# Performance work log

Hardware: AMD Instinct MI355X
Metric: run time of the kernel (lower is better)

The kernel has to match this reference:

```python
import jax, jax.numpy as jnp
import numpy as np
import math

D_MODEL = 768
N_HEAD = 12
D_FF = 3072
LN_EPS = 1e-5


def gelu_new(x):
    return 0.5 * x * (1.0 + jnp.tanh(jnp.sqrt(2.0 / jnp.pi) * (x + 0.044715 * x ** 3)))


def layer_norm(x, g, b):
    mu = jnp.mean(x, axis=-1, keepdims=True)
    var = jnp.mean(jnp.square(x - mu), axis=-1, keepdims=True)
    return (x - mu) * jax.lax.rsqrt(var + LN_EPS) * g + b


def setup_inputs() -> dict:
    key = jax.random.key(0)
    ks = jax.random.split(key, 8)
    B, S = 4, 2048
    x = jax.random.normal(ks[0], (B, S, D_MODEL), dtype=jnp.float32)
    # causal look-ahead mask: 1 = attend, 0 = masked
    look_ahead_mask = jnp.tril(jnp.ones((S, S), dtype=jnp.float32))[None, None]
    std = 0.02
    Wqkv = jax.random.normal(ks[1], (D_MODEL, 3 * D_MODEL), dtype=jnp.float32) * std
    bqkv = jnp.zeros((3 * D_MODEL,), dtype=jnp.float32)
    Wo = jax.random.normal(ks[2], (D_MODEL, D_MODEL), dtype=jnp.float32) * std
    bo = jnp.zeros((D_MODEL,), dtype=jnp.float32)
    Wfc = jax.random.normal(ks[3], (D_MODEL, D_FF), dtype=jnp.float32) * std
    bfc = jnp.zeros((D_FF,), dtype=jnp.float32)
    Wpr = jax.random.normal(ks[4], (D_FF, D_MODEL), dtype=jnp.float32) * std
    bpr = jnp.zeros((D_MODEL,), dtype=jnp.float32)
    g1 = jnp.ones((D_MODEL,), dtype=jnp.float32)
    b1 = jnp.zeros((D_MODEL,), dtype=jnp.float32)
    g2 = jnp.ones((D_MODEL,), dtype=jnp.float32)
    b2 = jnp.zeros((D_MODEL,), dtype=jnp.float32)
    return dict(x=x, look_ahead_mask=look_ahead_mask, Wqkv=Wqkv, bqkv=bqkv,
                Wo=Wo, bo=bo, Wfc=Wfc, bfc=bfc, Wpr=Wpr, bpr=bpr,
                g1=g1, b1=b1, g2=g2, b2=b2)


def reference(x, look_ahead_mask, Wqkv, bqkv, Wo, bo, Wfc, bfc, Wpr, bpr, g1, b1, g2, b2):
    B, S, D = x.shape
    dk = D // N_HEAD
    # --- attention sublayer (dropout = identity, eval mode) ---
    nx = layer_norm(x, g1, b1)
    qkv = nx @ Wqkv + bqkv                       # [B,S,3D]
    q, k, v = jnp.split(qkv, 3, axis=-1)
    def heads(t):
        return t.reshape(B, S, N_HEAD, dk).transpose(0, 2, 1, 3)  # [B,H,S,dk]
    q, k, v = heads(q), heads(k), heads(v)
    scores = jnp.einsum('bhqd,bhkd->bhqk', q, k) / jnp.sqrt(jnp.float32(dk))
    scores = scores + (1.0 - look_ahead_mask) * -10000.0
    attn_scores = jax.nn.softmax(scores, axis=-1)  # [B,H,S,S]
    out = jnp.einsum('bhqk,bhkd->bhqd', attn_scores, v)
    out = out.transpose(0, 2, 1, 3).reshape(B, S, D)
    a = out @ Wo + bo
    x = x + a
    # --- MLP sublayer ---
    h = layer_norm(x, g2, b2)
    m = gelu_new(h @ Wfc + bfc) @ Wpr + bpr
    x = x + m
    return (x, attn_scores)
```

## Files before the change

### kernel.cpp

```cpp
#include <hip/hip_runtime.h>
#include <stdint.h>

#define D_MODEL 768
#define NHEAD   12
#define DKH     64
#define SEQ     2048
#define BATCH   4
#define DFF     3072
#define NROWS   (BATCH*SEQ)

typedef __bf16 bf16x8 __attribute__((ext_vector_type(8)));
typedef float  f32x4  __attribute__((ext_vector_type(4)));

__device__ __forceinline__ unsigned short f2bf(float f) {
  union { float f; unsigned int u; } v; v.f = f;
  unsigned int r = v.u + 0x7fffu + ((v.u >> 16) & 1u);
  return (unsigned short)(r >> 16);
}

__device__ __forceinline__ void gl_lds16(const void* g, void* l) {
  __builtin_amdgcn_global_load_lds(
      (__attribute__((address_space(1))) void*)(uintptr_t)g,
      (__attribute__((address_space(3))) void*)(uintptr_t)l, 16, 0, 0);
}

__global__ __launch_bounds__(256) void k_wtrans_all(
    const float* __restrict__ Wqkv, const float* __restrict__ Wo,
    const float* __restrict__ Wfc, const float* __restrict__ Wpr,
    unsigned short* __restrict__ WqkvT, unsigned short* __restrict__ WoT,
    unsigned short* __restrict__ WfcT, unsigned short* __restrict__ WprT) {
  int id = blockIdx.x;
  const float* W; unsigned short* Wt; int K, N, tid;
  if (id < 1728)      { W = Wqkv; Wt = WqkvT; K = 768;  N = 2304; tid = id; }
  else if (id < 2304) { W = Wo;   Wt = WoT;   K = 768;  N = 768;  tid = id - 1728; }
  else if (id < 4608) { W = Wfc;  Wt = WfcT;  K = 768;  N = 3072; tid = id - 2304; }
  else                { W = Wpr;  Wt = WprT;  K = 3072; N = 768;  tid = id - 4608; }
  int ntn = N / 32;
  int n0 = (tid % ntn) * 32, k0 = (tid / ntn) * 32;

  __shared__ float tile[32][33];
  int c = threadIdx.x & 31, r = threadIdx.x >> 5;
#pragma unroll
  for (int i = 0; i < 4; ++i)
    tile[r + i * 8][c] = W[(size_t)(k0 + r + i * 8) * N + n0 + c];
  __syncthreads();
#pragma unroll
  for (int i = 0; i < 4; ++i)
    Wt[(size_t)(n0 + r + i * 8) * K + k0 + c] = f2bf(tile[c][r + i * 8]);
}

__global__ __launch_bounds__(256) void k_ln(const float* __restrict__ x,
                                            const float* __restrict__ g,
                                            const float* __restrict__ bb,
                                            unsigned short* __restrict__ y) {
  int row = blockIdx.x, t = threadIdx.x;
  const float* xr = x + (size_t)row * D_MODEL;
  float v0 = xr[t], v1 = xr[t + 256], v2 = xr[t + 512];
  float s = v0 + v1 + v2;
  float s2 = v0 * v0 + v1 * v1 + v2 * v2;
#pragma unroll
  for (int off = 32; off >= 1; off >>= 1) {
    s  += __shfl_xor(s, off, 64);
    s2 += __shfl_xor(s2, off, 64);
  }
  __shared__ float rs_[4], rs2_[4];
  int w = t >> 6;
  if ((t & 63) == 0) { rs_[w] = s; rs2_[w] = s2; }
  __syncthreads();
  s  = rs_[0] + rs_[1] + rs_[2] + rs_[3];
  s2 = rs2_[0] + rs2_[1] + rs2_[2] + rs2_[3];
  float mu  = s * (1.0f / D_MODEL);
  float var = s2 * (1.0f / D_MODEL) - mu * mu;
  float rstd = rsqrtf(var + 1e-5f);
  unsigned short* yr = y + (size_t)row * D_MODEL;
  yr[t]       = f2bf((v0 - mu) * rstd * g[t]       + bb[t]);
  yr[t + 256] = f2bf((v1 - mu) * rstd * g[t + 256] + bb[t + 256]);
  yr[t + 512] = f2bf((v2 - mu) * rstd * g[t + 512] + bb[t + 512]);
}

#define EPI_QKV 0
#define EPI_WO  1
#define EPI_FC  2
#define EPI_PR  3

template <int EPI>
__global__ __launch_bounds__(256) void k_gemm(
    const unsigned short* __restrict__ A,
    const unsigned short* __restrict__ Bt,
    const float* __restrict__ bias,
    const float* __restrict__ res,
    float* __restrict__ outf,
    unsigned short* __restrict__ outb,
    unsigned short* __restrict__ qo,
    unsigned short* __restrict__ ko,
    unsigned short* __restrict__ vto,
    int K, int N) {
  __shared__ __align__(16) unsigned char smem[36864];
  unsigned short* As = (unsigned short*)smem;
  unsigned short* Bs = (unsigned short*)(smem + 16384);
  int t = threadIdx.x;
  int l = t & 63, w = t >> 6;
  int wm = w >> 1, wn = w & 1;
  int m0 = blockIdx.y * 128, n0 = blockIdx.x * 128;
  int lr = l & 15, lg = l >> 4;

  const f32x4 fz = {0.0f, 0.0f, 0.0f, 0.0f};
  f32x4 acc[4][4];
#pragma unroll
  for (int i = 0; i < 4; ++i)
#pragma unroll
    for (int j = 0; j < 4; ++j) acc[i][j] = fz;

  int arow = t >> 3;
  int aslot = t & 7;
  const unsigned short* Ag = A + (size_t)(m0 + arow) * K + aslot * 8;
  const unsigned short* Bg = Bt + (size_t)(n0 + arow) * K + aslot * 8;
  int ntile = K >> 6;

  for (int kt = 0; kt < ntile; ++kt) {
    const unsigned short* Agk = Ag + kt * 64;
    const unsigned short* Bgk = Bg + kt * 64;
#pragma unroll
    for (int i = 0; i < 4; ++i)
      gl_lds16(Agk + (size_t)i * 32 * K, As + (i * 256 + t) * 8);
#pragma unroll
    for (int i = 0; i < 4; ++i)
      gl_lds16(Bgk + (size_t)i * 32 * K, Bs + (i * 256 + t) * 8);
    __syncthreads();
#pragma unroll
    for (int ks = 0; ks < 2; ++ks) {
      bf16x8 af[4], bf_[4];
#pragma unroll
      for (int i = 0; i < 4; ++i)
        af[i] = *(const bf16x8*)(As + (wm * 64 + i * 16 + lr) * 64 + ks * 32 + lg * 8);
#pragma unroll
      for (int i = 0; i < 4; ++i)
        bf_[i] = *(const bf16x8*)(Bs + (wn * 64 + i * 16 + lr) * 64 + ks * 32 + lg * 8);
#pragma unroll
      for (int i = 0; i < 4; ++i)
#pragma unroll
        for (int j = 0; j < 4; ++j)
          acc[i][j] = __builtin_amdgcn_mfma_f32_16x16x32_bf16(af[i], bf_[j], acc[i][j], 0, 0, 0);
    }
    __syncthreads();
  }

  int mb = m0 + wm * 64;
  int nb = n0 + wn * 64;

  if constexpr (EPI == EPI_WO || EPI == EPI_PR) {
#pragma unroll
    for (int i = 0; i < 4; ++i)
#pragma unroll
      for (int r = 0; r < 4; ++r) {
        int m = mb + i * 16 + 4 * lg + r;
#pragma unroll
        for (int j = 0; j < 4; ++j) {
          int n = nb + j * 16 + lr;
          outf[(size_t)m * D_MODEL + n] = acc[i][j][r] + bias[n] + res[(size_t)m * D_MODEL + n];
        }
      }
  } else if constexpr (EPI == EPI_FC) {
#pragma unroll
    for (int i = 0; i < 4; ++i)
#pragma unroll
      for (int r = 0; r < 4; ++r) {
        int m = mb + i * 16 + 4 * lg + r;
#pragma unroll
        for (int j = 0; j < 4; ++j) {
          int n = nb + j * 16 + lr;
          float u = acc[i][j][r] + bias[n];
          float c = 0.7978845608028654f * (u + 0.044715f * u * u * u);
          float a2 = fabsf(c);
          float e = __expf(-2.0f * a2);
          float th = (1.0f - e) / (1.0f + e);
          th = (c < 0.0f) ? -th : th;
          float gl = 0.5f * u * (1.0f + th);
          outb[(size_t)m * DFF + n] = f2bf(gl);
        }
      }
  } else {
    int region = n0 / 768;
    int b = m0 >> 11;
    if (region < 2) {
      unsigned short* dst = (region == 0) ? qo : ko;
#pragma unroll
      for (int i = 0; i < 4; ++i)
#pragma unroll
        for (int r = 0; r < 4; ++r) {
          int m = mb + i * 16 + 4 * lg + r;
          int s = m & (SEQ - 1);
#pragma unroll
          for (int j = 0; j < 4; ++j) {
            int n = nb + j * 16 + lr;
            int nl = n - region * 768;
            int h = nl >> 6, d = nl & 63;
            dst[(((size_t)(b * NHEAD + h) * SEQ + s) << 6) + d] = f2bf(acc[i][j][r] + bias[n]);
          }
        }
    } else {
      int nl = nb - 1536;
      int h = nl >> 6;
      unsigned short* Tw = (unsigned short*)(smem + w * 9216);
#pragma unroll
      for (int j = 0; j < 4; ++j) {
        int dcol = j * 16 + lr;
        int n = nb + j * 16 + lr;
#pragma unroll
        for (int i = 0; i < 4; ++i)
#pragma unroll
          for (int r = 0; r < 4; ++r)
            Tw[dcol * 72 + i * 16 + 4 * lg + r] = f2bf(acc[i][j][r] + bias[n]);
      }
      __syncthreads();
      int srow = l >> 3, sc = (l & 7) * 8;
      int s0 = mb & (SEQ - 1);
#pragma unroll
      for (int i = 0; i < 8; ++i) {
        int d = i * 8 + srow;
        bf16x8 vv = *(const bf16x8*)(Tw + d * 72 + sc);
        *(bf16x8*)(vto + ((size_t)(b * NHEAD + h) * DKH + d) * SEQ + s0 + sc) = vv;
      }
    }
  }
}

template <int WRITEP>
__global__ __launch_bounds__(256) void k_attn(const unsigned short* __restrict__ q,
                                              const unsigned short* __restrict__ kk,
                                              const unsigned short* __restrict__ vt,
                                              float* __restrict__ lsumbuf,
                                              float* __restrict__ attn,
                                              unsigned short* __restrict__ ao) {
  __shared__ __align__(16) unsigned short Ks[64 * 64];
  __shared__ __align__(16) unsigned short Vts[64 * 64];
  __shared__ __align__(16) unsigned short Pw[4][32 * 72];
  int t = threadIdx.x, l = t & 63, w = t >> 6;
  int lr = l & 15, lg = l >> 4;
  int qt = gridDim.x - 1 - blockIdx.x;
  int bh = blockIdx.y;
  int q0 = qt * 128;
  int qrow0 = q0 + w * 32;
  int kmax = 2 * qt + 1;

  bf16x8 aq[2][2];
#pragma unroll
  for (int m = 0; m < 2; ++m) {
    const unsigned short* qbase = q + ((size_t)bh * SEQ + qrow0 + m * 16 + lr) * DKH;
    aq[m][0] = *(const bf16x8*)(qbase + lg * 8);
    aq[m][1] = *(const bf16x8*)(qbase + 32 + lg * 8);
  }

  const f32x4 fz = {0.0f, 0.0f, 0.0f, 0.0f};
  float lsum[2][4] = {{0.f, 0.f, 0.f, 0.f}, {0.f, 0.f, 0.f, 0.f}};

  for (int kt = 0; kt <= kmax; ++kt) {
#pragma unroll
    for (int i = 0; i < 2; ++i) {
      int lin = i * 256 + t;
      gl_lds16(kk + ((size_t)bh * SEQ + kt * 64 + (lin >> 3)) * DKH + (lin & 7) * 8,
               Ks + lin * 8);
    }
    __syncthreads();
#pragma unroll
    for (int m = 0; m < 2; ++m) {
      f32x4 sacc[4];
#pragma unroll
      for (int f = 0; f < 4; ++f) sacc[f] = fz;
#pragma unroll
      for (int f = 0; f < 4; ++f) {
        bf16x8 bk0 = *(const bf16x8*)(Ks + (f * 16 + lr) * 64 + lg * 8);
        sacc[f] = __builtin_amdgcn_mfma_f32_16x16x32_bf16(aq[m][0], bk0, sacc[f], 0, 0, 0);
        bf16x8 bk1 = *(const bf16x8*)(Ks + (f * 16 + lr) * 64 + 32 + lg * 8);
        sacc[f] = __builtin_amdgcn_mfma_f32_16x16x32_bf16(aq[m][1], bk1, sacc[f], 0, 0, 0);
      }
#pragma unroll
      for (int r = 0; r < 4; ++r) {
        int qg = qrow0 + m * 16 + 4 * lg + r;
        float rsum = 0.f;
#pragma unroll
        for (int f = 0; f < 4; ++f) {
          int ksg = kt * 64 + f * 16 + lr;
          float p = (ksg <= qg) ? __expf(sacc[f][r] * 0.125f) : 0.0f;
          rsum += p;
        }
        rsum += __shfl_xor(rsum, 1, 64);
        rsum += __shfl_xor(rsum, 2, 64);
        rsum += __shfl_xor(rsum, 4, 64);
        rsum += __shfl_xor(rsum, 8, 64);
        lsum[m][r] += rsum;
      }
    }
    __syncthreads();
  }
  float invl[2][4];
#pragma unroll
  for (int m = 0; m < 2; ++m)
#pragma unroll
    for (int r = 0; r < 4; ++r) {
      invl[m][r] = 1.0f / lsum[m][r];
      if (WRITEP == 0 && lr == 0)
        lsumbuf[(size_t)bh * SEQ + qrow0 + m * 16 + 4 * lg + r] = lsum[m][r];
    }

  f32x4 oacc[2][4];
#pragma unroll
  for (int m = 0; m < 2; ++m)
#pragma unroll
    for (int f = 0; f < 4; ++f) oacc[m][f] = fz;

  unsigned short* Pme = Pw[w];
  for (int kt = 0; kt <= kmax; ++kt) {
#pragma unroll
    for (int i = 0; i < 2; ++i) {
      int lin = i * 256 + t;
      gl_lds16(kk + ((size_t)bh * SEQ + kt * 64 + (lin >> 3)) * DKH + (lin & 7) * 8,
               Ks + lin * 8);
      gl_lds16(vt + ((size_t)bh * DKH + (lin >> 3)) * SEQ + kt * 64 + (lin & 7) * 8,
               Vts + lin * 8);
    }
    __syncthreads();
#pragma unroll
    for (int m = 0; m < 2; ++m) {
      f32x4 sacc[4];
#pragma unroll
      for (int f = 0; f < 4; ++f) sacc[f] = fz;
#pragma unroll
      for (int f = 0; f < 4; ++f) {
        bf16x8 bk0 = *(const bf16x8*)(Ks + (f * 16 + lr) * 64 + lg * 8);
        sacc[f] = __builtin_amdgcn_mfma_f32_16x16x32_bf16(aq[m][0], bk0, sacc[f], 0, 0, 0);
        bf16x8 bk1 = *(const bf16x8*)(Ks + (f * 16 + lr) * 64 + 32 + lg * 8);
        sacc[f] = __builtin_amdgcn_mfma_f32_16x16x32_bf16(aq[m][1], bk1, sacc[f], 0, 0, 0);
      }
#pragma unroll
      for (int r = 0; r < 4; ++r) {
        int qg = qrow0 + m * 16 + 4 * lg + r;
#pragma unroll
        for (int f = 0; f < 4; ++f) {
          int ksg = kt * 64 + f * 16 + lr;
          float p = (ksg <= qg) ? __expf(sacc[f][r] * 0.125f) * invl[m][r] : 0.0f;
          if (WRITEP) attn[((size_t)bh * SEQ + qg) * SEQ + ksg] = p;
          Pme[(m * 16 + 4 * lg + r) * 72 + f * 16 + lr] = f2bf(p);
        }
      }
    }
#pragma unroll
    for (int ds = 0; ds < 2; ++ds)
#pragma unroll
      for (int m = 0; m < 2; ++m) {
        bf16x8 ap = *(const bf16x8*)(Pme + (m * 16 + lr) * 72 + ds * 32 + lg * 8);
#pragma unroll
        for (int f = 0; f < 4; ++f) {
          bf16x8 bv = *(const bf16x8*)(Vts + (f * 16 + lr) * 64 + ds * 32 + lg * 8);
          oacc[m][f] = __builtin_amdgcn_mfma_f32_16x16x32_bf16(ap, bv, oacc[m][f], 0, 0, 0);
        }
      }
    __syncthreads();
  }

  if (WRITEP) {
    int zstart = q0 + 128;
#pragma unroll
    for (int m = 0; m < 2; ++m)
#pragma unroll
      for (int r = 0; r < 4; ++r) {
        int qg = qrow0 + m * 16 + 4 * lg + r;
        float* rowp = attn + ((size_t)bh * SEQ + qg) * SEQ;
        for (int c = zstart + lr * 4; c < SEQ; c += 64)
          *(float4*)(rowp + c) = make_float4(0.f, 0.f, 0.f, 0.f);
      }
  }

  int b = bh / NHEAD, h = bh % NHEAD;
#pragma unroll
  for (int m = 0; m < 2; ++m)
#pragma unroll
    for (int r = 0; r < 4; ++r) {
      int qg = qrow0 + m * 16 + 4 * lg + r;
#pragma unroll
      for (int f = 0; f < 4; ++f)
        ao[(size_t)(b * SEQ + qg) * D_MODEL + h * DKH + f * 16 + lr] = f2bf(oacc[m][f][r]);
    }
}

__global__ __launch_bounds__(256) void k_pwrite(const unsigned short* __restrict__ q,
                                                const unsigned short* __restrict__ kk,
                                                const float* __restrict__ lsumbuf,
                                                float* __restrict__ attn) {
  __shared__ __align__(16) unsigned short Ks[64 * 64];
  int t = threadIdx.x, l = t & 63, w = t >> 6;
// ... 44 lines not shown

  int zstart = (qt + 1) * 64;
#pragma unroll
  for (int r = 0; r < 4; ++r) {
    int qg = qrow0 + 4 * lg + r;
    float* rowp = attn + ((size_t)bh * SEQ + qg) * SEQ;
    for (int c = zstart + lr * 4; c < SEQ; c += 64)
      *(float4*)(rowp + c) = make_float4(0.f, 0.f, 0.f, 0.f);
  }
}

extern "C" void kernel_launch(void* const* d_in, const int* in_sizes, int n_in,
                              void* d_out, int out_size, void* d_ws, size_t ws_size,
                              hipStream_t stream) {
  (void)in_sizes; (void)n_in; (void)out_size;
  const float* x    = (const float*)d_in[0];
  const float* Wqkv = (const float*)d_in[2];
  const float* bqkv = (const float*)d_in[3];
  const float* Wo   = (const float*)d_in[4];
  const float* bo   = (const float*)d_in[5];
  const float* Wfc  = (const float*)d_in[6];
  const float* bfc  = (const float*)d_in[7];
  const float* Wpr  = (const float*)d_in[8];
  const float* bpr  = (const float*)d_in[9];
  const float* g1   = (const float*)d_in[10];
  const float* b1   = (const float*)d_in[11];
  const float* g2   = (const float*)d_in[12];
  const float* b2   = (const float*)d_in[13];

  float* outx = (float*)d_out;
  float* attn = outx + (size_t)NROWS * D_MODEL;

  char* ws = (char*)d_ws;
  dim3 blk(256);

  const size_t NEED_FUSED = 77070336;
  if (ws_size >= NEED_FUSED + 65536) {
    unsigned short* qb    = (unsigned short*)(ws + 0);
    unsigned short* kb    = (unsigned short*)(ws + 12582912);
    unsigned short* vtb   = (unsigned short*)(ws + 25165824);
    unsigned short* m1    = (unsigned short*)(ws + 0);
    unsigned short* nx    = (unsigned short*)(ws + 50331648);
    unsigned short* ao    = (unsigned short*)(ws + 50331648);
    unsigned short* hb    = (unsigned short*)(ws + 50331648);
    unsigned short* WqkvT = (unsigned short*)(ws + 62914560);
    unsigned short* WoT   = (unsigned short*)(ws + 66453504);
    unsigned short* WfcT  = (unsigned short*)(ws + 67633152);
    unsigned short* WprT  = (unsigned short*)(ws + 72351744);
    float*          x1    = outx;

    k_wtrans_all<<<dim3(6912), blk, 0, stream>>>(Wqkv, Wo, Wfc, Wpr, WqkvT, WoT, WfcT, WprT);

    k_ln<<<NROWS, blk, 0, stream>>>(x, g1, b1, nx);

    k_gemm<EPI_QKV><<<dim3(2304 / 128, NROWS / 128), blk, 0, stream>>>(
        nx, WqkvT, bqkv, nullptr, nullptr, nullptr, qb, kb, vtb, 768, 2304);

    k_attn<1><<<dim3(SEQ / 128, BATCH * NHEAD), blk, 0, stream>>>(
        qb, kb, vtb, nullptr, attn, ao);

    k_gemm<EPI_WO><<<dim3(768 / 128, NROWS / 128), blk, 0, stream>>>(
        ao, WoT, bo, x, x1, nullptr, nullptr, nullptr, nullptr, 768, 768);

    k_ln<<<NROWS, blk, 0, stream>>>(x1, g2, b2, hb);

    k_gemm<EPI_FC><<<dim3(3072 / 128, NROWS / 128), blk, 0, stream>>>(
        hb, WfcT, bfc, nullptr, nullptr, m1, nullptr, nullptr, nullptr, 768, 3072);

    k_gemm<EPI_PR><<<dim3(768 / 128, NROWS / 128), blk, 0, stream>>>(
        m1, WprT, bpr, x1, outx, nullptr, nullptr, nullptr, nullptr, 3072, 768);
  } else {
    size_t off = 0;
    auto alloc = [&](size_t bytes) {
      char* p = ws + off;
      off += (bytes + 255) & ~(size_t)255;
      return p;
    };
    unsigned short* qb   = (unsigned short*)alloc((size_t)NROWS * D_MODEL * 2);
    unsigned short* kb   = (unsigned short*)alloc((size_t)NROWS * D_MODEL * 2);
    float*          lsum = (float*)alloc((size_t)BATCH * NHEAD * SEQ * 4);

    char* aws = (char*)attn;
    size_t aoff = 0;
    auto aalloc = [&](size_t bytes) {
      char* p = aws + aoff;
      aoff += (bytes + 255) & ~(size_t)255;
      return p;
    };
    unsigned short* WqkvT = (unsigned short*)aalloc((size_t)2304 * 768 * 2);
    unsigned short* WoT   = (unsigned short*)aalloc((size_t)768 * 768 * 2);
    unsigned short* WfcT  = (unsigned short*)aalloc((size_t)3072 * 768 * 2);
    unsigned short* WprT  = (unsigned short*)aalloc((size_t)768 * 3072 * 2);
    unsigned short* nx    = (unsigned short*)aalloc((size_t)NROWS * D_MODEL * 2);
    unsigned short* vtb   = (unsigned short*)aalloc((size_t)NROWS * D_MODEL * 2);
    unsigned short* ao    = (unsigned short*)aalloc((size_t)NROWS * D_MODEL * 2);
    float*          x1    = (float*)aalloc((size_t)NROWS * D_MODEL * 4);
    unsigned short* hb    = (unsigned short*)aalloc((size_t)NROWS * D_MODEL * 2);
    unsigned short* m1    = (unsigned short*)aalloc((size_t)NROWS * DFF * 2);

    k_wtrans_all<<<dim3(6912), blk, 0, stream>>>(Wqkv, Wo, Wfc, Wpr, WqkvT, WoT, WfcT, WprT);

    k_ln<<<NROWS, blk, 0, stream>>>(x, g1, b1, nx);

    k_gemm<EPI_QKV><<<dim3(2304 / 128, NROWS / 128), blk, 0, stream>>>(
        nx, WqkvT, bqkv, nullptr, nullptr, nullptr, qb, kb, vtb, 768, 2304);

    k_attn<0><<<dim3(SEQ / 128, BATCH * NHEAD), blk, 0, stream>>>(
        qb, kb, vtb, lsum, nullptr, ao);

    k_gemm<EPI_WO><<<dim3(768 / 128, NROWS / 128), blk, 0, stream>>>(
        ao, WoT, bo, x, x1, nullptr, nullptr, nullptr, nullptr, 768, 768);

    k_ln<<<NROWS, blk, 0, stream>>>(x1, g2, b2, hb);

    k_gemm<EPI_FC><<<dim3(3072 / 128, NROWS / 128), blk, 0, stream>>>(
        hb, WfcT, bfc, nullptr, nullptr, m1, nullptr, nullptr, nullptr, 768, 3072);

    k_gemm<EPI_PR><<<dim3(768 / 128, NROWS / 128), blk, 0, stream>>>(
        m1, WprT, bpr, x1, outx, nullptr, nullptr, nullptr, nullptr, 3072, 768);

    k_pwrite<<<dim3(SEQ / 64, BATCH * NHEAD), blk, 0, stream>>>(qb, kb, lsum, attn);
  }
}
```

Before: 605.9 us.

## Rewrite GEMM as 256x128 double-buffered 8-wave kernel with grid swizzle

```diff
diff --git a/kernel.cpp b/kernel.cpp
--- a/kernel.cpp
+++ b/kernel.cpp
@@ -83,8 +83,29 @@
 #define EPI_FC  2
 #define EPI_PR  3
 
+__device__ __forceinline__ void quad_mfma(const unsigned short* Ac, const unsigned short* Bc,
+                                          int qr, int qc, int wr64, int wc16, int lr, int lg,
+                                          f32x4* accq) {
+  bf16x8 a_[4][2], b_[2];
+#pragma unroll
+  for (int fi = 0; fi < 4; ++fi)
+#pragma unroll
+    for (int kk = 0; kk < 2; ++kk)
+      a_[fi][kk] = *(const bf16x8*)(Ac + (qr * 128 + wr64 + fi * 16 + lr) * 64 + kk * 32 + lg * 8);
+#pragma unroll
+  for (int kk = 0; kk < 2; ++kk)
+    b_[kk] = *(const bf16x8*)(Bc + (qc * 64 + wc16 + lr) * 64 + kk * 32 + lg * 8);
+  __builtin_amdgcn_s_setprio(1);
+#pragma unroll
+  for (int kk = 0; kk < 2; ++kk)
+#pragma unroll
+    for (int fi = 0; fi < 4; ++fi)
+      accq[fi] = __builtin_amdgcn_mfma_f32_16x16x32_bf16(a_[fi][kk], b_[kk], accq[fi], 0, 0, 0);
+  __builtin_amdgcn_s_setprio(0);
+}
+
 template <int EPI>
-__global__ __launch_bounds__(256) void k_gemm(
+__global__ __launch_bounds__(512, 2) void k_gemm2(
     const unsigned short* __restrict__ A,
     const unsigned short* __restrict__ Bt,
     const float* __restrict__ bias,
@@ -95,131 +116,159 @@
     unsigned short* __restrict__ ko,
     unsigned short* __restrict__ vto,
     int K, int N) {
-  __shared__ __align__(16) unsigned char smem[36864];
-  unsigned short* As = (unsigned short*)smem;
-  unsigned short* Bs = (unsigned short*)(smem + 16384);
+  __shared__ __align__(16) unsigned short smem[49152];
+
   int t = threadIdx.x;
   int l = t & 63, w = t >> 6;
-  int wm = w >> 1, wn = w & 1;
-  int m0 = blockIdx.y * 128, n0 = blockIdx.x * 128;
   int lr = l & 15, lg = l >> 4;
+  int wr64 = (w >> 2) * 64;
+  int wc16 = (w & 3) * 16;
+
+  int gx = gridDim.x, gy = gridDim.y;
+  int nwg = gx * gy;
+  int orig = blockIdx.y * gx + blockIdx.x;
+  int wg = (orig & 7) * (nwg >> 3) + (orig >> 3);
+  int bx = wg % gx, by = wg / gx;
+  int m0 = by * 256, n0 = bx * 128;
 
   const f32x4 fz = {0.0f, 0.0f, 0.0f, 0.0f};
   f32x4 acc[4][4];
 #pragma unroll
-  for (int i = 0; i < 4; ++i)
-#pragma unroll
-    for (int j = 0; j < 4; ++j) acc[i][j] = fz;
-
-  int arow = t >> 3;
-  int aslot = t & 7;
-  const unsigned short* Ag = A + (size_t)(m0 + arow) * K + aslot * 8;
-  const unsigned short* Bg = Bt + (size_t)(n0 + arow) * K + aslot * 8;
-  int ntile = K >> 6;
-
-  for (int kt = 0; kt < ntile; ++kt) {
-    const unsigned short* Agk = Ag + kt * 64;
-    const unsigned short* Bgk = Bg + kt * 64;
-#pragma unroll
-    for (int i = 0; i < 4; ++i)
-      gl_lds16(Agk + (size_t)i * 32 * K, As + (i * 256 + t) * 8);
-#pragma unroll
-    for (int i = 0; i < 4; ++i)
-      gl_lds16(Bgk + (size_t)i * 32 * K, Bs + (i * 256 + t) * 8);
-    __syncthreads();
-#pragma unroll
-    for (int ks = 0; ks < 2; ++ks) {
-      bf16x8 af[4], bf_[4];
-#pragma unroll
-      for (int i = 0; i < 4; ++i)
-        af[i] = *(const bf16x8*)(As + (wm * 64 + i * 16 + lr) * 64 + ks * 32 + lg * 8);
-#pragma unroll
-      for (int i = 0; i < 4; ++i)
-        bf_[i] = *(const bf16x8*)(Bs + (wn * 64 + i * 16 + lr) * 64 + ks * 32 + lg * 8);
-#pragma unroll
-      for (int i = 0; i < 4; ++i)
-#pragma unroll
-        for (int j = 0; j < 4; ++j)
-          acc[i][j] = __builtin_amdgcn_mfma_f32_16x16x32_bf16(af[i], bf_[j], acc[i][j], 0, 0, 0);
-    }
-    __syncthreads();
-  }
-
-  int mb = m0 + wm * 64;
-  int nb = n0 + wn * 64;
+  for (int q = 0; q < 4; ++q)
+#pragma unroll
+    for (int fi = 0; fi < 4; ++fi) acc[q][fi] = fz;
+
+  int trow = t >> 3, tcol = (t & 7) * 8;
+  int NT = K >> 6;
+
+  auto stageA = [&](unsigned short* As, int T, int hh) {
+#pragma unroll
+    for (int i = 0; i < 2; ++i)
+      gl_lds16(A + (size_t)(m0 + hh * 128 + i * 64 + trow) * K + T * 64 + tcol,
+               As + hh * 8192 + i * 4096 + t * 8);
+  };
+  auto stageB = [&](unsigned short* Bs, int T, int hh) {
+    gl_lds16(Bt + (size_t)(n0 + hh * 64 + trow) * K + T * 64 + tcol,
+             Bs + hh * 4096 + t * 8);
+  };
+
+  stageA(smem, 0, 0);
+  stageB(smem + 16384, 0, 0);
+  stageA(smem, 0, 1);
+  stageB(smem + 16384, 0, 1);
+
+  for (int T = 0; T < NT; ++T) {
+    int cur = T & 1;
+    unsigned short* Ac = smem + cur * 24576;
+    unsigned short* Bc = Ac + 16384;
+    unsigned short* An = smem + (cur ^ 1) * 24576;
+    unsigned short* Bn = An + 16384;
+    bool pf = (T + 1 < NT);
+
+    asm volatile("s_waitcnt lgkmcnt(0)" ::: "memory");
+    asm volatile("s_waitcnt vmcnt(3)" ::: "memory");
+    __builtin_amdgcn_s_barrier();
+    asm volatile("" ::: "memory");
+    if (pf) stageA(An, T + 1, 0);
+    quad_mfma(Ac, Bc, 0, 0, wr64, wc16, lr, lg, acc[0]);
+
+    asm volatile("s_waitcnt lgkmcnt(0)" ::: "memory");
+    if (pf) asm volatile("s_waitcnt vmcnt(2)" ::: "memory");
+    else    asm volatile("s_waitcnt vmcnt(0)" ::: "memory");
+    __builtin_amdgcn_s_barrier();
+    asm volatile("" ::: "memory");
+    if (pf) stageB(Bn, T + 1, 0);
+    quad_mfma(Ac, Bc, 0, 1, wr64, wc16, lr, lg, acc[1]);
+
+    if (pf) stageA(An, T + 1, 1);
+    quad_mfma(Ac, Bc, 1, 1, wr64, wc16, lr, lg, acc[2]);
+
+    if (pf) stageB(Bn, T + 1, 1);
+    quad_mfma(Ac, Bc, 1, 0, wr64, wc16, lr, lg, acc[3]);
+  }
 
   if constexpr (EPI == EPI_WO || EPI == EPI_PR) {
 #pragma unroll
-    for (int i = 0; i < 4; ++i)
-#pragma unroll
-      for (int r = 0; r < 4; ++r) {
-        int m = mb + i * 16 + 4 * lg + r;
-#pragma unroll
-        for (int j = 0; j < 4; ++j) {
-          int n = nb + j * 16 + lr;
-          outf[(size_t)m * D_MODEL + n] = acc[i][j][r] + bias[n] + res[(size_t)m * D_MODEL + n];
+    for (int q = 0; q < 4; ++q) {
+      int qr = q >> 1, qc = (q == 1 || q == 2) ? 1 : 0;
+#pragma unroll
+      for (int fi = 0; fi < 4; ++fi)
+#pragma unroll
+        for (int r = 0; r < 4; ++r) {
+          int m = m0 + qr * 128 + wr64 + fi * 16 + 4 * lg + r;
+          int n = n0 + qc * 64 + wc16 + lr;
+          outf[(size_t)m * N + n] = acc[q][fi][r] + bias[n] + res[(size_t)m * N + n];
         }
-      }
+    }
   } else if constexpr (EPI == EPI_FC) {
 #pragma unroll
-    for (int i = 0; i < 4; ++i)
-#pragma unroll
-      for (int r = 0; r < 4; ++r) {
-        int m = mb + i * 16 + 4 * lg + r;
-#pragma unroll
-        for (int j = 0; j < 4; ++j) {
-          int n = nb + j * 16 + lr;
-          float u = acc[i][j][r] + bias[n];
+    for (int q = 0; q < 4; ++q) {
+      int qr = q >> 1, qc = (q == 1 || q == 2) ? 1 : 0;
+#pragma unroll
+      for (int fi = 0; fi < 4; ++fi)
+#pragma unroll
+        for (int r = 0; r < 4; ++r) {
+          int m = m0 + qr * 128 + wr64 + fi * 16 + 4 * lg + r;
+          int n = n0 + qc * 64 + wc16 + lr;
+          float u = acc[q][fi][r] + bias[n];
           float c = 0.7978845608028654f * (u + 0.044715f * u * u * u);
           float a2 = fabsf(c);
           float e = __expf(-2.0f * a2);
           float th = (1.0f - e) / (1.0f + e);
           th = (c < 0.0f) ? -th : th;
-          float gl = 0.5f * u * (1.0f + th);
-          outb[(size_t)m * DFF + n] = f2bf(gl);
+          outb[(size_t)m * N + n] = f2bf(0.5f * u * (1.0f + th));
         }
-      }
+    }
   } else {
     int region = n0 / 768;
     int b = m0 >> 11;
     if (region < 2) {
       unsigned short* dst = (region == 0) ? qo : ko;
 #pragma unroll
-      for (int i = 0; i < 4; ++i)
-#pragma unroll
-        for (int r = 0; r < 4; ++r) {
-          int m = mb + i * 16 + 4 * lg + r;
-          int s = m & (SEQ - 1);
-#pragma unroll
-          for (int j = 0; j < 4; ++j) {
-            int n = nb + j * 16 + lr;
+      for (int q = 0; q < 4; ++q) {
+        int qr = q >> 1, qc = (q == 1 || q == 2) ? 1 : 0;
+#pragma unroll
+        for (int fi = 0; fi < 4; ++fi)
+#pragma unroll
+          for (int r = 0; r < 4; ++r) {
+            int m = m0 + qr * 128 + wr64 + fi * 16 + 4 * lg + r;
+            int n = n0 + qc * 64 + wc16 + lr;
+            int s = m & (SEQ - 1);
             int nl = n - region * 768;
             int h = nl >> 6, d = nl & 63;
-            dst[(((size_t)(b * NHEAD + h) * SEQ + s) << 6) + d] = f2bf(acc[i][j][r] + bias[n]);
+            dst[(((size_t)(b * NHEAD + h) * SEQ + s) << 6) + d] = f2bf(acc[q][fi][r] + bias[n]);
+          }
+      }
+    } else {
+      __syncthreads();
+      unsigned short* Tw = smem + w * 4096;
+#pragma unroll
+      for (int q = 0; q < 4; ++q) {
+        int qr = q >> 1, qc = (q == 1 || q == 2) ? 1 : 0;
+#pragma unroll
+        for (int fi = 0; fi < 4; ++fi)
+#pragma unroll
+          for (int r = 0; r < 4; ++r) {
+            int n = n0 + qc * 64 + wc16 + lr;
+            Tw[qc * 2048 + lr * 128 + qr * 64 + fi * 16 + 4 * lg + r] =
+                f2bf(acc[q][fi][r] + bias[n]);
+          }
+      }
+      int hbase = (n0 - 1536) >> 6;
+#pragma unroll
+      for (int qc = 0; qc < 2; ++qc) {
+        int h = hbase + qc;
+#pragma unroll
+        for (int qr = 0; qr < 2; ++qr) {
+          int sbase = m0 + qr * 128 + wr64;
+          int s0 = sbase & (SEQ - 1);
+#pragma unroll
+          for (int i = 0; i < 2; ++i) {
+            int dloc = i * 8 + (l >> 3);
+            bf16x8 vv = *(const bf16x8*)(Tw + qc * 2048 + dloc * 128 + qr * 64 + (l & 7) * 8);
+            *(bf16x8*)(vto + ((size_t)(b * NHEAD + h) * DKH + wc16 + dloc) * SEQ + s0 + (l & 7) * 8) = vv;
           }
         }
-    } else {
-      int nl = nb - 1536;
-      int h = nl >> 6;
-      unsigned short* Tw = (unsigned short*)(smem + w * 9216);
-#pragma unroll
-      for (int j = 0; j < 4; ++j) {
-        int dcol = j * 16 + lr;
-        int n = nb + j * 16 + lr;
-#pragma unroll
-        for (int i = 0; i < 4; ++i)
-#pragma unroll
-          for (int r = 0; r < 4; ++r)
-            Tw[dcol * 72 + i * 16 + 4 * lg + r] = f2bf(acc[i][j][r] + bias[n]);
-      }
-      __syncthreads();
-      int srow = l >> 3, sc = (l & 7) * 8;
-      int s0 = mb & (SEQ - 1);
-#pragma unroll
-      for (int i = 0; i < 8; ++i) {
-        int d = i * 8 + srow;
-        bf16x8 vv = *(const bf16x8*)(Tw + d * 72 + sc);
-        *(bf16x8*)(vto + ((size_t)(b * NHEAD + h) * DKH + d) * SEQ + s0 + sc) = vv;
       }
     }
   }
@@ -466,7 +515,7 @@
   float* attn = outx + (size_t)NROWS * D_MODEL;
 
   char* ws = (char*)d_ws;
-  dim3 blk(256);
+  dim3 blk(256), blkg(512);
 
   const size_t NEED_FUSED = 77070336;
   if (ws_size >= NEED_FUSED + 65536) {
@@ -484,24 +533,17 @@
     float*          x1    = outx;
 
     k_wtrans_all<<<dim3(6912), blk, 0, stream>>>(Wqkv, Wo, Wfc, Wpr, WqkvT, WoT, WfcT, WprT);
-
     k_ln<<<NROWS, blk, 0, stream>>>(x, g1, b1, nx);
-
-    k_gemm<EPI_QKV><<<dim3(2304 / 128, NROWS / 128), blk, 0, stream>>>(
+    k_gemm2<EPI_QKV><<<dim3(18, 32), blkg, 0, stream>>>(
         nx, WqkvT, bqkv, nullptr, nullptr, nullptr, qb, kb, vtb, 768, 2304);
-
     k_attn<1><<<dim3(SEQ / 128, BATCH * NHEAD), blk, 0, stream>>>(
         qb, kb, vtb, nullptr, attn, ao);
-
-    k_gemm<EPI_WO><<<dim3(768 / 128, NROWS / 128), blk, 0, stream>>>(
+    k_gemm2<EPI_WO><<<dim3(6, 32), blkg, 0, stream>>>(
         ao, WoT, bo, x, x1, nullptr, nullptr, nullptr, nullptr, 768, 768);
-
     k_ln<<<NROWS, blk, 0, stream>>>(x1, g2, b2, hb);
-
-    k_gemm<EPI_FC><<<dim3(3072 / 128, NROWS / 128), blk, 0, stream>>>(
+    k_gemm2<EPI_FC><<<dim3(24, 32), blkg, 0, stream>>>(
         hb, WfcT, bfc, nullptr, nullptr, m1, nullptr, nullptr, nullptr, 768, 3072);
-
-    k_gemm<EPI_PR><<<dim3(768 / 128, NROWS / 128), blk, 0, stream>>>(
+    k_gemm2<EPI_PR><<<dim3(6, 32), blkg, 0, stream>>>(
         m1, WprT, bpr, x1, outx, nullptr, nullptr, nullptr, nullptr, 3072, 768);
   } else {
     size_t off = 0;
@@ -533,24 +575,17 @@
     unsigned short* m1    = (unsigned short*)aalloc((size_t)NROWS * DFF * 2);
 
     k_wtrans_all<<<dim3(6912), blk, 0, stream>>>(Wqkv, Wo, Wfc, Wpr, WqkvT, WoT, WfcT, WprT);
-
     k_ln<<<NROWS, blk, 0, stream>>>(x, g1, b1, nx);
-
-    k_gemm<EPI_QKV><<<dim3(2304 / 128, NROWS / 128), blk, 0, stream>>>(
+    k_gemm2<EPI_QKV><<<dim3(18, 32), blkg, 0, stream>>>(
         nx, WqkvT, bqkv, nullptr, nullptr, nullptr, qb, kb, vtb, 768, 2304);
-
     k_attn<0><<<dim3(SEQ / 128, BATCH * NHEAD), blk, 0, stream>>>(
         qb, kb, vtb, lsum, nullptr, ao);
-
-    k_gemm<EPI_WO><<<dim3(768 / 128, NROWS / 128), blk, 0, stream>>>(
+    k_gemm2<EPI_WO><<<dim3(6, 32), blkg, 0, stream>>>(
         ao, WoT, bo, x, x1, nullptr, nullptr, nullptr, nullptr, 768, 768);
-
     k_ln<<<NROWS, blk, 0, stream>>>(x1, g2, b2, hb);
-
-    k_gemm<EPI_FC><<<dim3(3072 / 128, NROWS / 128), blk, 0, stream>>>(
+    k_gemm2<EPI_FC><<<dim3(24, 32), blkg, 0, stream>>>(
         hb, WfcT, bfc, nullptr, nullptr, m1, nullptr, nullptr, nullptr, 768, 3072);
-
-    k_gemm<EPI_PR><<<dim3(768 / 128, NROWS / 128), blk, 0, stream>>>(
+    k_gemm2<EPI_PR><<<dim3(6, 32), blkg, 0, stream>>>(
         m1, WprT, bpr, x1, outx, nullptr, nullptr, nullptr, nullptr, 3072, 768);
 
     k_pwrite<<<dim3(SEQ / 64, BATCH * NHEAD), blk, 0, stream>>>(qb, kb, lsum, attn);
```

Measured after the change: 738.9 us. 21.9% more time.

## Load attention K/V tiles straight from global memory into registers, dropping LDS staging

Applied to the files above, without the earlier changes.

```diff
diff --git a/kernel.cpp b/kernel.cpp
--- a/kernel.cpp
+++ b/kernel.cpp
@@ -175,8 +175,7 @@
           float e = __expf(-2.0f * a2);
           float th = (1.0f - e) / (1.0f + e);
           th = (c < 0.0f) ? -th : th;
-          float gl = 0.5f * u * (1.0f + th);
-          outb[(size_t)m * DFF + n] = f2bf(gl);
+          outb[(size_t)m * DFF + n] = f2bf(0.5f * u * (1.0f + th));
         }
       }
   } else {
@@ -232,13 +231,11 @@
                                               float* __restrict__ lsumbuf,
                                               float* __restrict__ attn,
                                               unsigned short* __restrict__ ao) {
-  __shared__ __align__(16) unsigned short Ks[64 * 64];
-  __shared__ __align__(16) unsigned short Vts[64 * 64];
   __shared__ __align__(16) unsigned short Pw[4][32 * 72];
   int t = threadIdx.x, l = t & 63, w = t >> 6;
   int lr = l & 15, lg = l >> 4;
-  int qt = gridDim.x - 1 - blockIdx.x;
-  int bh = blockIdx.y;
+  int bh = blockIdx.x;
+  int qt = gridDim.y - 1 - blockIdx.y;
   int q0 = qt * 128;
   int qrow0 = q0 + w * 32;
   int kmax = 2 * qt + 1;
@@ -253,15 +250,17 @@
 
   const f32x4 fz = {0.0f, 0.0f, 0.0f, 0.0f};
   float lsum[2][4] = {{0.f, 0.f, 0.f, 0.f}, {0.f, 0.f, 0.f, 0.f}};
+  const unsigned short* Kbh = kk + (size_t)bh * SEQ * DKH;
+  const unsigned short* Vbh = vt + (size_t)bh * DKH * SEQ;
 
   for (int kt = 0; kt <= kmax; ++kt) {
-#pragma unroll
-    for (int i = 0; i < 2; ++i) {
-      int lin = i * 256 + t;
-      gl_lds16(kk + ((size_t)bh * SEQ + kt * 64 + (lin >> 3)) * DKH + (lin & 7) * 8,
-               Ks + lin * 8);
-    }
-    __syncthreads();
+    const unsigned short* Kt = Kbh + (size_t)kt * 64 * DKH;
+    bf16x8 bk[4][2];
+#pragma unroll
+    for (int f = 0; f < 4; ++f) {
+      bk[f][0] = *(const bf16x8*)(Kt + (f * 16 + lr) * 64 + lg * 8);
+      bk[f][1] = *(const bf16x8*)(Kt + (f * 16 + lr) * 64 + 32 + lg * 8);
+    }
 #pragma unroll
     for (int m = 0; m < 2; ++m) {
       f32x4 sacc[4];
@@ -269,10 +268,8 @@
       for (int f = 0; f < 4; ++f) sacc[f] = fz;
 #pragma unroll
       for (int f = 0; f < 4; ++f) {
-        bf16x8 bk0 = *(const bf16x8*)(Ks + (f * 16 + lr) * 64 + lg * 8);
-        sacc[f] = __builtin_amdgcn_mfma_f32_16x16x32_bf16(aq[m][0], bk0, sacc[f], 0, 0, 0);
-        bf16x8 bk1 = *(const bf16x8*)(Ks + (f * 16 + lr) * 64 + 32 + lg * 8);
-        sacc[f] = __builtin_amdgcn_mfma_f32_16x16x32_bf16(aq[m][1], bk1, sacc[f], 0, 0, 0);
+        sacc[f] = __builtin_amdgcn_mfma_f32_16x16x32_bf16(aq[m][0], bk[f][0], sacc[f], 0, 0, 0);
+        sacc[f] = __builtin_amdgcn_mfma_f32_16x16x32_bf16(aq[m][1], bk[f][1], sacc[f], 0, 0, 0);
       }
 #pragma unroll
       for (int r = 0; r < 4; ++r) {
@@ -291,7 +288,6 @@
         lsum[m][r] += rsum;
       }
     }
-    __syncthreads();
   }
   float invl[2][4];
 #pragma unroll
@@ -311,15 +307,13 @@
 
   unsigned short* Pme = Pw[w];
   for (int kt = 0; kt <= kmax; ++kt) {
-#pragma unroll
-    for (int i = 0; i < 2; ++i) {
-      int lin = i * 256 + t;
-      gl_lds16(kk + ((size_t)bh * SEQ + kt * 64 + (lin >> 3)) * DKH + (lin & 7) * 8,
-               Ks + lin * 8);
-      gl_lds16(vt + ((size_t)bh * DKH + (lin >> 3)) * SEQ + kt * 64 + (lin & 7) * 8,
-               Vts + lin * 8);
-    }
-    __syncthreads();
+    const unsigned short* Kt = Kbh + (size_t)kt * 64 * DKH;
+    bf16x8 bk[4][2];
+#pragma unroll
+    for (int f = 0; f < 4; ++f) {
+      bk[f][0] = *(const bf16x8*)(Kt + (f * 16 + lr) * 64 + lg * 8);
+      bk[f][1] = *(const bf16x8*)(Kt + (f * 16 + lr) * 64 + 32 + lg * 8);
+    }
 #pragma unroll
     for (int m = 0; m < 2; ++m) {
       f32x4 sacc[4];
@@ -327,10 +321,8 @@
       for (int f = 0; f < 4; ++f) sacc[f] = fz;
 #pragma unroll
       for (int f = 0; f < 4; ++f) {
-        bf16x8 bk0 = *(const bf16x8*)(Ks + (f * 16 + lr) * 64 + lg * 8);
-        sacc[f] = __builtin_amdgcn_mfma_f32_16x16x32_bf16(aq[m][0], bk0, sacc[f], 0, 0, 0);
-        bf16x8 bk1 = *(const bf16x8*)(Ks + (f * 16 + lr) * 64 + 32 + lg * 8);
-        sacc[f] = __builtin_amdgcn_mfma_f32_16x16x32_bf16(aq[m][1], bk1, sacc[f], 0, 0, 0);
+        sacc[f] = __builtin_amdgcn_mfma_f32_16x16x32_bf16(aq[m][0], bk[f][0], sacc[f], 0, 0, 0);
+        sacc[f] = __builtin_amdgcn_mfma_f32_16x16x32_bf16(aq[m][1], bk[f][1], sacc[f], 0, 0, 0);
       }
 #pragma unroll
       for (int r = 0; r < 4; ++r) {
@@ -345,17 +337,19 @@
       }
     }
 #pragma unroll
-    for (int ds = 0; ds < 2; ++ds)
+    for (int ds = 0; ds < 2; ++ds) {
+      bf16x8 bv[4];
+#pragma unroll
+      for (int f = 0; f < 4; ++f)
+        bv[f] = *(const bf16x8*)(Vbh + (size_t)(f * 16 + lr) * SEQ + kt * 64 + ds * 32 + lg * 8);
 #pragma unroll
       for (int m = 0; m < 2; ++m) {
         bf16x8 ap = *(const bf16x8*)(Pme + (m * 16 + lr) * 72 + ds * 32 + lg * 8);
 #pragma unroll
-        for (int f = 0; f < 4; ++f) {
-          bf16x8 bv = *(const bf16x8*)(Vts + (f * 16 + lr) * 64 + ds * 32 + lg * 8);
-          oacc[m][f] = __builtin_amdgcn_mfma_f32_16x16x32_bf16(ap, bv, oacc[m][f], 0, 0, 0);
-        }
-      }
-    __syncthreads();
+        for (int f = 0; f < 4; ++f)
+          oacc[m][f] = __builtin_amdgcn_mfma_f32_16x16x32_bf16(ap, bv[f], oacc[m][f], 0, 0, 0);
+      }
+    }
   }
 
   if (WRITEP) {
@@ -484,24 +478,17 @@
     float*          x1    = outx;
 
     k_wtrans_all<<<dim3(6912), blk, 0, stream>>>(Wqkv, Wo, Wfc, Wpr, WqkvT, WoT, WfcT, WprT);
-
     k_ln<<<NROWS, blk, 0, stream>>>(x, g1, b1, nx);
-
-    k_gemm<EPI_QKV><<<dim3(2304 / 128, NROWS / 128), blk, 0, stream>>>(
+    k_gemm<EPI_QKV><<<dim3(18, 64), blk, 0, stream>>>(
         nx, WqkvT, bqkv, nullptr, nullptr, nullptr, qb, kb, vtb, 768, 2304);
-
-    k_attn<1><<<dim3(SEQ / 128, BATCH * NHEAD), blk, 0, stream>>>(
+    k_attn<1><<<dim3(BATCH * NHEAD, SEQ / 128), blk, 0, stream>>>(
         qb, kb, vtb, nullptr, attn, ao);
-
-    k_gemm<EPI_WO><<<dim3(768 / 128, NROWS / 128), blk, 0, stream>>>(
+    k_gemm<EPI_WO><<<dim3(6, 64), blk, 0, stream>>>(
         ao, WoT, bo, x, x1, nullptr, nullptr, nullptr, nullptr, 768, 768);
-
     k_ln<<<NROWS, blk, 0, stream>>>(x1, g2, b2, hb);
-
-    k_gemm<EPI_FC><<<dim3(3072 / 128, NROWS / 128), blk, 0, stream>>>(
+    k_gemm<EPI_FC><<<dim3(24, 64), blk, 0, stream>>>(
         hb, WfcT, bfc, nullptr, nullptr, m1, nullptr, nullptr, nullptr, 768, 3072);
-
-    k_gemm<EPI_PR><<<dim3(768 / 128, NROWS / 128), blk, 0, stream>>>(
+    k_gemm<EPI_PR><<<dim3(6, 64), blk, 0, stream>>>(
         m1, WprT, bpr, x1, outx, nullptr, nullptr, nullptr, nullptr, 3072, 768);
   } else {
     size_t off = 0;
@@ -533,24 +520,17 @@
     unsigned short* m1    = (unsigned short*)aalloc((size_t)NROWS * DFF * 2);
 
     k_wtrans_all<<<dim3(6912), blk, 0, stream>>>(Wqkv, Wo, Wfc, Wpr, WqkvT, WoT, WfcT, WprT);
-
     k_ln<<<NROWS, blk, 0, stream>>>(x, g1, b1, nx);
-
-    k_gemm<EPI_QKV><<<dim3(2304 / 128, NROWS / 128), blk, 0, stream>>>(
+    k_gemm<EPI_QKV><<<dim3(18, 64), blk, 0, stream>>>(
         nx, WqkvT, bqkv, nullptr, nullptr, nullptr, qb, kb, vtb, 768, 2304);
-
-    k_attn<0><<<dim3(SEQ / 128, BATCH * NHEAD), blk, 0, stream>>>(
+    k_attn<0><<<dim3(BATCH * NHEAD, SEQ / 128), blk, 0, stream>>>(
         qb, kb, vtb, lsum, nullptr, ao);
-
-    k_gemm<EPI_WO><<<dim3(768 / 128, NROWS / 128), blk, 0, stream>>>(
+    k_gemm<EPI_WO><<<dim3(6, 64), blk, 0, stream>>>(
         ao, WoT, bo, x, x1, nullptr, nullptr, nullptr, nullptr, 768, 768);
-
     k_ln<<<NROWS, blk, 0, stream>>>(x1, g2, b2, hb);
-
-    k_gemm<EPI_FC><<<dim3(3072 / 128, NROWS / 128), blk, 0, stream>>>(
+    k_gemm<EPI_FC><<<dim3(24, 64), blk, 0, stream>>>(
         hb, WfcT, bfc, nullptr, nullptr, m1, nullptr, nullptr, nullptr, 768, 3072);
-
-    k_gemm<EPI_PR><<<dim3(768 / 128, NROWS / 128), blk, 0, stream>>>(
+    k_gemm<EPI_PR><<<dim3(6, 64), blk, 0, stream>>>(
         m1, WprT, bpr, x1, outx, nullptr, nullptr, nullptr, nullptr, 3072, 768);
 
     k_pwrite<<<dim3(SEQ / 64, BATCH * NHEAD), blk, 0, stream>>>(qb, kb, lsum, attn);
```

Result: slower. 631.5 us (+4.2%).

## Double-buffer K/V tiles in attention and fuse first LayerNorm into weight prep

Applied to the files above, without the earlier changes.

```diff
diff --git a/kernel.cpp b/kernel.cpp
--- a/kernel.cpp
+++ b/kernel.cpp
@@ -24,29 +24,58 @@
       (__attribute__((address_space(3))) void*)(uintptr_t)l, 16, 0, 0);
 }
 
-__global__ __launch_bounds__(256) void k_wtrans_all(
+__global__ __launch_bounds__(256) void k_prep(
     const float* __restrict__ Wqkv, const float* __restrict__ Wo,
     const float* __restrict__ Wfc, const float* __restrict__ Wpr,
     unsigned short* __restrict__ WqkvT, unsigned short* __restrict__ WoT,
-    unsigned short* __restrict__ WfcT, unsigned short* __restrict__ WprT) {
+    unsigned short* __restrict__ WfcT, unsigned short* __restrict__ WprT,
+    const float* __restrict__ x, const float* __restrict__ g1,
+    const float* __restrict__ b1, unsigned short* __restrict__ nx) {
   int id = blockIdx.x;
-  const float* W; unsigned short* Wt; int K, N, tid;
-  if (id < 1728)      { W = Wqkv; Wt = WqkvT; K = 768;  N = 2304; tid = id; }
-  else if (id < 2304) { W = Wo;   Wt = WoT;   K = 768;  N = 768;  tid = id - 1728; }
-  else if (id < 4608) { W = Wfc;  Wt = WfcT;  K = 768;  N = 3072; tid = id - 2304; }
-  else                { W = Wpr;  Wt = WprT;  K = 3072; N = 768;  tid = id - 4608; }
-  int ntn = N / 32;
-  int n0 = (tid % ntn) * 32, k0 = (tid / ntn) * 32;
-
-  __shared__ float tile[32][33];
-  int c = threadIdx.x & 31, r = threadIdx.x >> 5;
-#pragma unroll
-  for (int i = 0; i < 4; ++i)
-    tile[r + i * 8][c] = W[(size_t)(k0 + r + i * 8) * N + n0 + c];
-  __syncthreads();
-#pragma unroll
-  for (int i = 0; i < 4; ++i)
-    Wt[(size_t)(n0 + r + i * 8) * K + k0 + c] = f2bf(tile[c][r + i * 8]);
+  if (id < NROWS) {
+    int row = id, t = threadIdx.x;
+    const float* xr = x + (size_t)row * D_MODEL;
+    float v0 = xr[t], v1 = xr[t + 256], v2 = xr[t + 512];
+    float s = v0 + v1 + v2;
+    float s2 = v0 * v0 + v1 * v1 + v2 * v2;
+#pragma unroll
+    for (int off = 32; off >= 1; off >>= 1) {
+      s  += __shfl_xor(s, off, 64);
+      s2 += __shfl_xor(s2, off, 64);
+    }
+    __shared__ float rs_[4], rs2_[4];
+    int w = t >> 6;
+    if ((t & 63) == 0) { rs_[w] = s; rs2_[w] = s2; }
+    __syncthreads();
+    s  = rs_[0] + rs_[1] + rs_[2] + rs_[3];
+    s2 = rs2_[0] + rs2_[1] + rs2_[2] + rs2_[3];
+    float mu  = s * (1.0f / D_MODEL);
+    float var = s2 * (1.0f / D_MODEL) - mu * mu;
+    float rstd = rsqrtf(var + 1e-5f);
+    unsigned short* yr = nx + (size_t)row * D_MODEL;
+    yr[t]       = f2bf((v0 - mu) * rstd * g1[t]       + b1[t]);
+    yr[t + 256] = f2bf((v1 - mu) * rstd * g1[t + 256] + b1[t + 256]);
+    yr[t + 512] = f2bf((v2 - mu) * rstd * g1[t + 512] + b1[t + 512]);
+  } else {
+    int wid = id - NROWS;
+    const float* W; unsigned short* Wt; int K, N, tid;
+    if (wid < 1728)      { W = Wqkv; Wt = WqkvT; K = 768;  N = 2304; tid = wid; }
+    else if (wid < 2304) { W = Wo;   Wt = WoT;   K = 768;  N = 768;  tid = wid - 1728; }
+    else if (wid < 4608) { W = Wfc;  Wt = WfcT;  K = 768;  N = 3072; tid = wid - 2304; }
+    else                 { W = Wpr;  Wt = WprT;  K = 3072; N = 768;  tid = wid - 4608; }
+    int ntn = N / 32;
+    int n0 = (tid % ntn) * 32, k0 = (tid / ntn) * 32;
+
+    __shared__ float tile[32][33];
+    int c = threadIdx.x & 31, r = threadIdx.x >> 5;
+#pragma unroll
+    for (int i = 0; i < 4; ++i)
+      tile[r + i * 8][c] = W[(size_t)(k0 + r + i * 8) * N + n0 + c];
+    __syncthreads();
+#pragma unroll
+    for (int i = 0; i < 4; ++i)
+      Wt[(size_t)(n0 + r + i * 8) * K + k0 + c] = f2bf(tile[c][r + i * 8]);
+  }
 }
 
 __global__ __launch_bounds__(256) void k_ln(const float* __restrict__ x,
@@ -175,8 +204,7 @@
           float e = __expf(-2.0f * a2);
           float th = (1.0f - e) / (1.0f + e);
           th = (c < 0.0f) ? -th : th;
-          float gl = 0.5f * u * (1.0f + th);
-          outb[(size_t)m * DFF + n] = f2bf(gl);
+          outb[(size_t)m * DFF + n] = f2bf(0.5f * u * (1.0f + th));
         }
       }
   } else {
@@ -232,8 +260,8 @@
                                               float* __restrict__ lsumbuf,
                                               float* __restrict__ attn,
                                               unsigned short* __restrict__ ao) {
-  __shared__ __align__(16) unsigned short Ks[64 * 64];
-  __shared__ __align__(16) unsigned short Vts[64 * 64];
+  __shared__ __align__(16) unsigned short Ks[2][64 * 64];
+  __shared__ __align__(16) unsigned short Vts[2][64 * 64];
   __shared__ __align__(16) unsigned short Pw[4][32 * 72];
   int t = threadIdx.x, l = t & 63, w = t >> 6;
   int lr = l & 15, lg = l >> 4;
@@ -243,6 +271,23 @@
   int qrow0 = q0 + w * 32;
   int kmax = 2 * qt + 1;
 
+  auto stageK = [&](int kt, int buf) {
+#pragma unroll
+    for (int i = 0; i < 2; ++i) {
+      int lin = i * 256 + t;
+      gl_lds16(kk + ((size_t)bh * SEQ + kt * 64 + (lin >> 3)) * DKH + (lin & 7) * 8,
+               Ks[buf] + lin * 8);
+    }
+  };
+  auto stageV = [&](int kt, int buf) {
+#pragma unroll
+    for (int i = 0; i < 2; ++i) {
+      int lin = i * 256 + t;
+      gl_lds16(vt + ((size_t)bh * DKH + (lin >> 3)) * SEQ + kt * 64 + (lin & 7) * 8,
+               Vts[buf] + lin * 8);
+    }
+  };
+
   bf16x8 aq[2][2];
 #pragma unroll
   for (int m = 0; m < 2; ++m) {
@@ -254,14 +299,12 @@
   const f32x4 fz = {0.0f, 0.0f, 0.0f, 0.0f};
   float lsum[2][4] = {{0.f, 0.f, 0.f, 0.f}, {0.f, 0.f, 0.f, 0.f}};
 
+  stageK(0, 0);
+  __syncthreads();
+  int cur = 0;
   for (int kt = 0; kt <= kmax; ++kt) {
-#pragma unroll
-    for (int i = 0; i < 2; ++i) {
-      int lin = i * 256 + t;
-      gl_lds16(kk + ((size_t)bh * SEQ + kt * 64 + (lin >> 3)) * DKH + (lin & 7) * 8,
-               Ks + lin * 8);
-    }
-    __syncthreads();
+    if (kt < kmax) stageK(kt + 1, cur ^ 1);
+    const unsigned short* Kc = Ks[cur];
 #pragma unroll
     for (int m = 0; m < 2; ++m) {
       f32x4 sacc[4];
@@ -269,9 +312,9 @@
       for (int f = 0; f < 4; ++f) sacc[f] = fz;
 #pragma unroll
       for (int f = 0; f < 4; ++f) {
-        bf16x8 bk0 = *(const bf16x8*)(Ks + (f * 16 + lr) * 64 + lg * 8);
+        bf16x8 bk0 = *(const bf16x8*)(Kc + (f * 16 + lr) * 64 + lg * 8);
         sacc[f] = __builtin_amdgcn_mfma_f32_16x16x32_bf16(aq[m][0], bk0, sacc[f], 0, 0, 0);
-        bf16x8 bk1 = *(const bf16x8*)(Ks + (f * 16 + lr) * 64 + 32 + lg * 8);
+        bf16x8 bk1 = *(const bf16x8*)(Kc + (f * 16 + lr) * 64 + 32 + lg * 8);
         sacc[f] = __builtin_amdgcn_mfma_f32_16x16x32_bf16(aq[m][1], bk1, sacc[f], 0, 0, 0);
       }
 #pragma unroll
@@ -292,6 +335,7 @@
       }
     }
     __syncthreads();
+    cur ^= 1;
   }
   float invl[2][4];
 #pragma unroll
@@ -310,16 +354,14 @@
     for (int f = 0; f < 4; ++f) oacc[m][f] = fz;
 
   unsigned short* Pme = Pw[w];
+  stageK(0, 0);
+  stageV(0, 0);
+  __syncthreads();
+  cur = 0;
   for (int kt = 0; kt <= kmax; ++kt) {
-#pragma unroll
-    for (int i = 0; i < 2; ++i) {
-      int lin = i * 256 + t;
-      gl_lds16(kk + ((size_t)bh * SEQ + kt * 64 + (lin >> 3)) * DKH + (lin & 7) * 8,
-               Ks + lin * 8);
-      gl_lds16(vt + ((size_t)bh * DKH + (lin >> 3)) * SEQ + kt * 64 + (lin & 7) * 8,
-               Vts + lin * 8);
-    }
-    __syncthreads();
+    if (kt < kmax) { stageK(kt + 1, cur ^ 1); stageV(kt + 1, cur ^ 1); }
+    const unsigned short* Kc = Ks[cur];
+    const unsigned short* Vc = Vts[cur];
 #pragma unroll
     for (int m = 0; m < 2; ++m) {
       f32x4 sacc[4];
@@ -327,9 +369,9 @@
       for (int f = 0; f < 4; ++f) sacc[f] = fz;
 #pragma unroll
       for (int f = 0; f < 4; ++f) {
-        bf16x8 bk0 = *(const bf16x8*)(Ks + (f * 16 + lr) * 64 + lg * 8);
+        bf16x8 bk0 = *(const bf16x8*)(Kc + (f * 16 + lr) * 64 + lg * 8);
         sacc[f] = __builtin_amdgcn_mfma_f32_16x16x32_bf16(aq[m][0], bk0, sacc[f], 0, 0, 0);
-        bf16x8 bk1 = *(const bf16x8*)(Ks + (f * 16 + lr) * 64 + 32 + lg * 8);
+        bf16x8 bk1 = *(const bf16x8*)(Kc + (f * 16 + lr) * 64 + 32 + lg * 8);
         sacc[f] = __builtin_amdgcn_mfma_f32_16x16x32_bf16(aq[m][1], bk1, sacc[f], 0, 0, 0);
       }
 #pragma unroll
@@ -351,11 +393,12 @@
         bf16x8 ap = *(const bf16x8*)(Pme + (m * 16 + lr) * 72 + ds * 32 + lg * 8);
 #pragma unroll
         for (int f = 0; f < 4; ++f) {
-          bf16x8 bv = *(const bf16x8*)(Vts + (f * 16 + lr) * 64 + ds * 32 + lg * 8);
+          bf16x8 bv = *(const bf16x8*)(Vc + (f * 16 + lr) * 64 + ds * 32 + lg * 8);
           oacc[m][f] = __builtin_amdgcn_mfma_f32_16x16x32_bf16(ap, bv, oacc[m][f], 0, 0, 0);
         }
       }
     __syncthreads();
+    cur ^= 1;
   }
 
   if (WRITEP) {
@@ -483,25 +526,18 @@
     unsigned short* WprT  = (unsigned short*)(ws + 72351744);
     float*          x1    = outx;
 
-    k_wtrans_all<<<dim3(6912), blk, 0, stream>>>(Wqkv, Wo, Wfc, Wpr, WqkvT, WoT, WfcT, WprT);
-
-    k_ln<<<NROWS, blk, 0, stream>>>(x, g1, b1, nx);
-
-    k_gemm<EPI_QKV><<<dim3(2304 / 128, NROWS / 128), blk, 0, stream>>>(
+    k_prep<<<dim3(NROWS + 6912), blk, 0, stream>>>(
+        Wqkv, Wo, Wfc, Wpr, WqkvT, WoT, WfcT, WprT, x, g1, b1, nx);
+    k_gemm<EPI_QKV><<<dim3(18, 64), blk, 0, stream>>>(
         nx, WqkvT, bqkv, nullptr, nullptr, nullptr, qb, kb, vtb, 768, 2304);
-
     k_attn<1><<<dim3(SEQ / 128, BATCH * NHEAD), blk, 0, stream>>>(
         qb, kb, vtb, nullptr, attn, ao);
-
-    k_gemm<EPI_WO><<<dim3(768 / 128, NROWS / 128), blk, 0, stream>>>(
+    k_gemm<EPI_WO><<<dim3(6, 64), blk, 0, stream>>>(
         ao, WoT, bo, x, x1, nullptr, nullptr, nullptr, nullptr, 768, 768);
-
     k_ln<<<NROWS, blk, 0, stream>>>(x1, g2, b2, hb);
-
-    k_gemm<EPI_FC><<<dim3(3072 / 128, NROWS / 128), blk, 0, stream>>>(
+    k_gemm<EPI_FC><<<dim3(24, 64), blk, 0, stream>>>(
         hb, WfcT, bfc, nullptr, nullptr, m1, nullptr, nullptr, nullptr, 768, 3072);
-
-    k_gemm<EPI_PR><<<dim3(768 / 128, NROWS / 128), blk, 0, stream>>>(
+    k_gemm<EPI_PR><<<dim3(6, 64), blk, 0, stream>>>(
         m1, WprT, bpr, x1, outx, nullptr, nullptr, nullptr, nullptr, 3072, 768);
   } else {
     size_t off = 0;
@@ -532,25 +568,18 @@
     unsigned short* hb    = (unsigned short*)aalloc((size_t)NROWS * D_MODEL * 2);
     unsigned short* m1    = (unsigned short*)aalloc((size_t)NROWS * DFF * 2);
 
-    k_wtrans_all<<<dim3(6912), blk, 0, stream>>>(Wqkv, Wo, Wfc, Wpr, WqkvT, WoT, WfcT, WprT);
-
-    k_ln<<<NROWS, blk, 0, stream>>>(x, g1, b1, nx);
-
-    k_gemm<EPI_QKV><<<dim3(2304 / 128, NROWS / 128), blk, 0, stream>>>(
+    k_prep<<<dim3(NROWS + 6912), blk, 0, stream>>>(
+        Wqkv, Wo, Wfc, Wpr, WqkvT, WoT, WfcT, WprT, x, g1, b1, nx);
+    k_gemm<EPI_QKV><<<dim3(18, 64), blk, 0, stream>>>(
         nx, WqkvT, bqkv, nullptr, nullptr, nullptr, qb, kb, vtb, 768, 2304);
-
     k_attn<0><<<dim3(SEQ / 128, BATCH * NHEAD), blk, 0, stream>>>(
         qb, kb, vtb, lsum, nullptr, ao);
-
-    k_gemm<EPI_WO><<<dim3(768 / 128, NROWS / 128), blk, 0, stream>>>(
+    k_gemm<EPI_WO><<<dim3(6, 64), blk, 0, stream>>>(
         ao, WoT, bo, x, x1, nullptr, nullptr, nullptr, nullptr, 768, 768);
-
     k_ln<<<NROWS, blk, 0, stream>>>(x1, g2, b2, hb);
-
-    k_gemm<EPI_FC><<<dim3(3072 / 128, NROWS / 128), blk, 0, stream>>>(
+    k_gemm<EPI_FC><<<dim3(24, 64), blk, 0, stream>>>(
         hb, WfcT, bfc, nullptr, nullptr, m1, nullptr, nullptr, nullptr, 768, 3072);
-
-    k_gemm<EPI_PR><<<dim3(768 / 128, NROWS / 128), blk, 0, stream>>>(
+    k_gemm<EPI_PR><<<dim3(6, 64), blk, 0, stream>>>(
         m1, WprT, bpr, x1, outx, nullptr, nullptr, nullptr, nullptr, 3072, 768);
 
     k_pwrite<<<dim3(SEQ / 64, BATCH * NHEAD), blk, 0, stream>>>(qb, kb, lsum, attn);
```

New measurement: 574.3 us. 1.06x faster.
